# Kernel tuning notes

Hardware: AMD Instinct MI355X
Metric: run time of the kernel (lower is better)

The kernel has to match this reference:

```python
import jax, jax.numpy as jnp
import numpy as np

B, T, C = 2, 2048, 1024
H = 16


def setup_inputs() -> dict:
    key = jax.random.key(0)
    k1, k2, k3 = jax.random.split(key, 3)
    X = jax.random.normal(k1, (B, T, C), dtype=jnp.float32)
    # scale weights like typical inits to keep activations sane
    W_qkv = jax.random.normal(k2, (C, 3 * C), dtype=jnp.float32) / np.sqrt(C)
    W_proj = jax.random.normal(k3, (C, C), dtype=jnp.float32) / np.sqrt(C)
    return {"X": X, "W_qkv": W_qkv, "W_proj": W_proj}


def reference(X, W_qkv, W_proj):
    b, t, c = X.shape
    hd = c // H  # head dim
    qkv = X @ W_qkv  # (B,T,3C)
    q, k, v = jnp.split(qkv, 3, axis=2)
    # (B,H,T,hd)
    q = q.reshape(b, t, H, hd).transpose(0, 2, 1, 3)
    k = k.reshape(b, t, H, hd).transpose(0, 2, 1, 3)
    v = v.reshape(b, t, H, hd).transpose(0, 2, 1, 3)
    att = jnp.einsum("bhqd,bhkd->bhqk", q, k) * (1.0 / np.sqrt(hd))
    causal = jnp.tril(jnp.ones((t, t), dtype=bool))[None, None]
    att = jnp.where(causal, att, -jnp.inf)
    att = jax.nn.softmax(att, axis=-1)
    y = jnp.einsum("bhqk,bhkd->bhqd", att, v)
    y = y.transpose(0, 2, 1, 3).reshape(b, t, c)
    return y @ W_proj
```

## Files before the change

### kernel.cpp

```cpp
#include <hip/hip_runtime.h>
#include <hip/hip_bf16.h>

typedef __attribute__((ext_vector_type(8))) short bf16x8;
typedef __attribute__((ext_vector_type(4))) float f32x4;

#define LOG2E 1.4426950408889634f

__device__ __forceinline__ unsigned short f2b(float f) {
  union { float f; unsigned u; } v; v.f = f;
  unsigned r = v.u + 0x7fffu + ((v.u >> 16) & 1u);
  return (unsigned short)(r >> 16);
}

__device__ __forceinline__ unsigned pack2(float a, float b) {
  __hip_bfloat162 h = __float22bfloat162_rn(make_float2(a, b));
  union { __hip_bfloat162 h; unsigned u; } v;
  v.h = h;
  return v.u;
}

__global__ void cast_x_kernel(const float* __restrict__ X, unsigned short* __restrict__ Xb, int n4) {
  int i = blockIdx.x * blockDim.x + threadIdx.x;
  if (i < n4) {
    float4 v = reinterpret_cast<const float4*>(X)[i];
    ushort4 o = make_ushort4(f2b(v.x), f2b(v.y), f2b(v.z), f2b(v.w));
    reinterpret_cast<ushort4*>(Xb)[i] = o;
  }
}

__global__ void transpose_cast_kernel(const float* __restrict__ W, unsigned short* __restrict__ Wt,
                                      int K, int N) {
  int lane = threadIdx.x & 63;
  int wave = threadIdx.x >> 6;
  int n = blockIdx.x * 64 + lane;
  int k0 = blockIdx.y * 32 + wave * 8;
  bf16x8 v;
#pragma unroll
  for (int j = 0; j < 8; ++j) v[j] = (short)f2b(W[(size_t)(k0 + j) * N + n]);
  *reinterpret_cast<bf16x8*>(&Wt[(size_t)n * K + k0]) = v;
}

__device__ __forceinline__ void stage_tile(const unsigned short* __restrict__ A,
                                           const unsigned short* __restrict__ Bt,
                                           int m0, int n0, int kk, int K,
                                           unsigned short* As, unsigned short* Bs, int tid) {
  int wave = tid >> 6;
  int row = tid >> 2;
  int chunk = tid & 3;
  typedef __attribute__((address_space(3))) unsigned int lds_u32;
  typedef const __attribute__((address_space(1))) unsigned int glb_u32;
  const unsigned short* ga0 = A + (size_t)(m0 + row) * K + kk + chunk * 8;
  const unsigned short* ga1 = A + (size_t)(m0 + 64 + row) * K + kk + chunk * 8;
  const unsigned short* gb0 = Bt + (size_t)(n0 + row) * K + kk + chunk * 8;
  const unsigned short* gb1 = Bt + (size_t)(n0 + 64 + row) * K + kk + chunk * 8;
  __builtin_amdgcn_global_load_lds((glb_u32*)ga0, (lds_u32*)(As + wave * 512), 16, 0, 0);
  __builtin_amdgcn_global_load_lds((glb_u32*)ga1, (lds_u32*)(As + 2048 + wave * 512), 16, 0, 0);
  __builtin_amdgcn_global_load_lds((glb_u32*)gb0, (lds_u32*)(Bs + wave * 512), 16, 0, 0);
  __builtin_amdgcn_global_load_lds((glb_u32*)gb1, (lds_u32*)(Bs + 2048 + wave * 512), 16, 0, 0);
}

template <int MODE>
__launch_bounds__(256, 2)
__global__ void gemm_bt_kernel(const unsigned short* __restrict__ A,
                               const unsigned short* __restrict__ Bt,
                               void* __restrict__ Cout,
                               unsigned short* __restrict__ Vt,
                               int M, int N, int K) {
  __shared__ __align__(16) unsigned short As[2][128 * 32];
  __shared__ __align__(16) unsigned short Bs[2][128 * 32];
  const int tid = threadIdx.x;
  const int lane = tid & 63;
  const int wave = tid >> 6;
  const int wr = wave >> 1, wc = wave & 1;
  const int m0 = blockIdx.y * 128;
  const int n0 = blockIdx.x * 128;
  const int lr = lane & 15;
  const int lk = (lane >> 4) * 8;

  f32x4 zero = {0.f, 0.f, 0.f, 0.f};
  f32x4 acc[4][4];
#pragma unroll
  for (int i = 0; i < 4; ++i)
#pragma unroll
    for (int j = 0; j < 4; ++j) acc[i][j] = zero;

  const int KT = K >> 5;
  stage_tile(A, Bt, m0, n0, 0, K, As[0], Bs[0], tid);
  int buf = 0;
  for (int kt = 0; kt < KT; ++kt) {
    __syncthreads();
    if (kt + 1 < KT) stage_tile(A, Bt, m0, n0, (kt + 1) << 5, K, As[buf ^ 1], Bs[buf ^ 1], tid);
    bf16x8 af[4], bfr[4];
#pragma unroll
    for (int mf = 0; mf < 4; ++mf)
      af[mf] = *reinterpret_cast<const bf16x8*>(&As[buf][(wr * 64 + mf * 16 + lr) * 32 + lk]);
#pragma unroll
    for (int nf = 0; nf < 4; ++nf)
      bfr[nf] = *reinterpret_cast<const bf16x8*>(&Bs[buf][(wc * 64 + nf * 16 + lr) * 32 + lk]);
#pragma unroll
    for (int mf = 0; mf < 4; ++mf)
#pragma unroll
      for (int nf = 0; nf < 4; ++nf)
        acc[mf][nf] = __builtin_amdgcn_mfma_f32_16x16x32_bf16(af[mf], bfr[nf], acc[mf][nf], 0, 0, 0);
    buf ^= 1;
  }

  const int lj = (lane >> 4) * 4;
  if (MODE == 1) {
    float* C = (float*)Cout;
#pragma unroll
    for (int mf = 0; mf < 4; ++mf)
#pragma unroll
      for (int nf = 0; nf < 4; ++nf) {
        int n = n0 + wc * 64 + nf * 16 + lr;
#pragma unroll
        for (int j = 0; j < 4; ++j) {
          int m = m0 + wr * 64 + mf * 16 + lj + j;
          C[(size_t)m * N + n] = acc[mf][nf][j];
        }
      }
  } else {
    unsigned short* QK = (unsigned short*)Cout;
    if (n0 < 2048) {
#pragma unroll
      for (int mf = 0; mf < 4; ++mf)
#pragma unroll
        for (int nf = 0; nf < 4; ++nf) {
          int n = n0 + wc * 64 + nf * 16 + lr;
          float scale = (n < 1024) ? 0.125f : 1.0f;
#pragma unroll
          for (int j = 0; j < 4; ++j) {
            int m = m0 + wr * 64 + mf * 16 + lj + j;
            QK[(size_t)m * 2048 + n] = f2b(acc[mf][nf][j] * scale);
          }
        }
    } else {
#pragma unroll
      for (int mf = 0; mf < 4; ++mf)
#pragma unroll
        for (int nf = 0; nf < 4; ++nf) {
          int n = n0 - 2048 + wc * 64 + nf * 16 + lr;
          int d = n & 63, h = n >> 6;
          int mbase = m0 + wr * 64 + mf * 16 + lj;
          int bb = mbase >> 11, t = mbase & 2047;
          ushort4 v = make_ushort4(f2b(acc[mf][nf][0]), f2b(acc[mf][nf][1]),
                                   f2b(acc[mf][nf][2]), f2b(acc[mf][nf][3]));
          *reinterpret_cast<ushort4*>(&Vt[(((size_t)bb * 16 + h) * 64 + d) * 2048 + t]) = v;
        }
    }
  }
}

#define PFENCE() asm volatile("s_waitcnt lgkmcnt(0)" ::: "memory")

#define KLOAD(TK)                                                                                 \
  {                                                                                               \
    const unsigned short* kp = Kbase + (size_t)((TK) << 6) * 2048;                                \
    _Pragma("unroll")                                                                             \
    for (int nf = 0; nf < 4; ++nf) {                                                              \
      const unsigned short* kq = kp + (size_t)(nf * 16) * 2048;                                   \
      kf[nf][0] = *reinterpret_cast<const bf16x8*>(kq);                                           \
      kf[nf][1] = *reinterpret_cast<const bf16x8*>(kq + 32);                                      \
    }                                                                                             \
  }

#define VLOADX(VF, TK)                                                                            \
  {                                                                                               \
    const unsigned short* vp0 = Vbase + ((TK) << 6);                                              \
    _Pragma("unroll")                                                                             \
    for (int mf = 0; mf < 4; ++mf) {                                                              \
      const unsigned short* vp = vp0 + (size_t)(mf * 16) * 2048;                                  \
      VF[mf][0] = *reinterpret_cast<const bf16x8*>(vp);                                           \
      VF[mf][1] = *reinterpret_cast<const bf16x8*>(vp + 32);                                      \
    }                                                                                             \
  }

#define QKC(ST, QF)                                                                               \
  {                                                                                               \
    __builtin_amdgcn_s_setprio(1);                                                                \
    _Pragma("unroll")                                                                             \
    for (int nf = 0; nf < 4; ++nf) {                                                              \
      ST[nf] = __builtin_amdgcn_mfma_f32_16x16x32_bf16(kf[nf][0], QF[0], zero, 0, 0, 0);          \
      ST[nf] = __builtin_amdgcn_mfma_f32_16x16x32_bf16(kf[nf][1], QF[1], ST[nf], 0, 0, 0);        \
    }                                                                                             \
    __builtin_amdgcn_s_setprio(0);                                                                \
  }

#define MASKST(ST, NFD)                                                                           \
  {                                                                                               \
    _Pragma("unroll")                                                                             \
    for (int nf = 0; nf < 4; ++nf)                                                                \
      _Pragma("unroll")                                                                           \
      for (int j = 0; j < 4; ++j) {                                                               \
        bool kill = (nf > (NFD)) || ((nf == (NFD)) && (4 * lhi + j > lr));                        \
        ST[nf][j] = kill ? -1e30f : ST[nf][j];                                                    \
      }                                                                                           \
  }

#define SMP(ST, MROW, LSUM, ACCO, WOUT)                                                           \
  {                                                                                               \
    float pmax = -1e30f;                                                                          \
    _Pragma("unroll")                                                                             \
    for (int nf = 0; nf < 4; ++nf)                                                                \
      _Pragma("unroll")                                                                           \
      for (int j = 0; j < 4; ++j) pmax = fmaxf(pmax, ST[nf][j]);                                  \
    pmax = fmaxf(pmax, __shfl_xor(pmax, 16));                                                     \
    pmax = fmaxf(pmax, __shfl_xor(pmax, 32));                                                     \
    const float mnew = fmaxf(MROW, pmax);                                                         \
    const float fsc = exp2f((MROW - mnew) * LOG2E);                                               \
    float psum = 0.f;                                                                             \
    _Pragma("unroll")                                                                             \
    for (int nf = 0; nf < 4; ++nf)                                                                \
      _Pragma("unroll")                                                                           \
      for (int h2 = 0; h2 < 2; ++h2) {                                                            \
        float p0 = exp2f((ST[nf][2 * h2] - mnew) * LOG2E);                                        \
        float p1 = exp2f((ST[nf][2 * h2 + 1] - mnew) * LOG2E);                                    \
        psum += p0 + p1;                                                                          \
        WOUT[nf * 2 + h2] = pack2(p0, p1);                                                        \
      }                                                                                           \
    psum += __shfl_xor(psum, 16);                                                                 \
    psum += __shfl_xor(psum, 32);                                                                 \
    LSUM = LSUM * fsc + psum;                                                                     \
    MROW = mnew;                                                                                  \
    _Pragma("unroll")                                                                             \
    for (int mf = 0; mf < 4; ++mf)                                                                \
      _Pragma("unroll")                                                                           \
      for (int j = 0; j < 4; ++j) ACCO[mf][j] *= fsc;                                             \
  }

#define PWRITE(PW, WIN)                                                                           \
  {                                                                                               \
    uint4 w0 = make_uint4(WIN[0], WIN[1], WIN[2], WIN[3]);                                        \
    uint4 w1 = make_uint4(WIN[4], WIN[5], WIN[6], WIN[7]);                                        \
    *reinterpret_cast<uint4*>(&PW[lr][8 * lhi]) = w0;                                             \
    *reinterpret_cast<uint4*>(&PW[lr][8 * lhi + 4]) = w1;                                         \
  }

#define PREAD(PW, PB)                                                                             \
  {                                                                                               \
    _Pragma("unroll")                                                                             \
    for (int kd = 0; kd < 2; ++kd) {                                                              \
      const int nfk = 2 * kd + (lhi >> 1);                                                        \
      const int c = 2 * (nfk & 1) + 4 * (nfk >> 1);                                               \
      const int s0 = 8 * ((2 * lhi) & 3) + c;                                                     \
      const int s1 = 8 * ((2 * lhi + 1) & 3) + c;                                                 \
      union { bf16x8 v; unsigned int u[4]; } pu;                                                  \
      uint2 ra = *reinterpret_cast<const uint2*>(&PW[lr][s0]);                                    \
      uint2 rb = *reinterpret_cast<const uint2*>(&PW[lr][s1]);                                    \
      pu.u[0] = ra.x; pu.u[1] = ra.y; pu.u[2] = rb.x; pu.u[3] = rb.y;                             \
      PB[kd] = pu.v;                                                                              \
    }                                                                                             \
  }

#define PVC(ACCO, VF, PB)                                                                         \
  {                                                                                               \
    __builtin_amdgcn_s_setprio(1);                                                                \
    _Pragma("unroll")                                                                             \
    for (int mf = 0; mf < 4; ++mf) {                                                              \
      ACCO[mf] = __builtin_amdgcn_mfma_f32_16x16x32_bf16(VF[mf][0], PB[0], ACCO[mf], 0, 0, 0);    \
      ACCO[mf] = __builtin_amdgcn_mfma_f32_16x16x32_bf16(VF[mf][1], PB[1], ACCO[mf], 0, 0, 0);    \
    }                                                                                             \
    __builtin_amdgcn_s_setprio(0);                                                                \
  }

#define EPILOG(ACCO, LSUM, Q0)                                                                    \
  {                                                                                               \
    const float inv = 1.0f / LSUM;                                                                \
    unsigned short* Op = O + ((size_t)(b * T + (Q0) + lr)) * 1024 + h * 64 + 4 * lhi;             \
    _Pragma("unroll")                                                                             \
    for (int mf = 0; mf < 4; ++mf) {                                                              \
      uint2 o = make_uint2(pack2(ACCO[mf][0] * inv, ACCO[mf][1] * inv),                           \
                           pack2(ACCO[mf][2] * inv, ACCO[mf][3] * inv));                          \
      *reinterpret_cast<uint2*>(Op + 16 * mf) = o;                                                \
    }                                                                                             \
  }

__launch_bounds__(64)
__global__ void attn_kernel(const unsigned short* __restrict__ QK,
                            const unsigned short* __restrict__ Vt,
                            unsigned short* __restrict__ O) {
  __shared__ unsigned int Pw[2][2][16][36];
  const int T = 2048;
  const int lane = threadIdx.x;
  const int lr = lane & 15;
  const int lhi = lane >> 4;
  const int bh = blockIdx.x & 31;
  const int pid = blockIdx.x >> 5;
  const int b = bh >> 4, h = bh & 15;
  const int qsA = 127 - pid, qsB = pid;
  const int q0A = qsA * 16, q0B = qsB * 16;
  const int ktmaxA = qsA >> 2, ktmaxB = qsB >> 2;
  const int nfdA = qsA & 3, nfdB = qsB & 3;

  const f32x4 zero = {0.f, 0.f, 0.f, 0.f};

  const unsigned short* QpA = QK + ((size_t)(b * T + q0A + lr)) * 2048 + h * 64 + lhi * 8;
  const unsigned short* QpB = QK + ((size_t)(b * T + q0B + lr)) * 2048 + h * 64 + lhi * 8;
  bf16x8 qfA[2] = {*reinterpret_cast<const bf16x8*>(QpA),
                   *reinterpret_cast<const bf16x8*>(QpA + 32)};
  bf16x8 qfB[2] = {*reinterpret_cast<const bf16x8*>(QpB),
                   *reinterpret_cast<const bf16x8*>(QpB + 32)};

  const unsigned short* Kbase = QK + ((size_t)(b * T + lr)) * 2048 + 1024 + h * 64 + lhi * 8;
  const unsigned short* Vbase = Vt + ((size_t)(bh * 64 + lr)) * 2048 + lhi * 8;

  bf16x8 kf[4][2];
  KLOAD(0);

  f32x4 accA[4] = {zero, zero, zero, zero};
  f32x4 accB[4] = {zero, zero, zero, zero};
  float mrowA = -1e30f, lsumA = 0.f, mrowB = -1e30f, lsumB = 0.f;

  for (int kt = 0; kt <= ktmaxA; ++kt) {
    const bool actB = (kt <= ktmaxB);
    const int pp = kt & 1;
    bf16x8 vf[4][2];
    VLOADX(vf, kt);

    f32x4 stA[4], stB[4];
    QKC(stA, qfA);
    if (actB) QKC(stB, qfB);
    {
      int tk = (kt + 1 > ktmaxA) ? ktmaxA : kt + 1;
      KLOAD(tk);
    }
    if (kt == ktmaxA) MASKST(stA, nfdA);
    if (actB && kt == ktmaxB) MASKST(stB, nfdB);

    unsigned WA[8], WB[8];
    SMP(stA, mrowA, lsumA, accA, WA);
    if (actB) SMP(stB, mrowB, lsumB, accB, WB);

    PWRITE(Pw[0][pp], WA);
    if (actB) PWRITE(Pw[1][pp], WB);
    PFENCE();
    bf16x8 pbA[2], pbB[2];
    PREAD(Pw[0][pp], pbA);
    if (actB) PREAD(Pw[1][pp], pbB);

    PVC(accA, vf, pbA);
    if (actB) PVC(accB, vf, pbB);
  }

  EPILOG(accA, lsumA, q0A);
  EPILOG(accB, lsumB, q0B);
}

extern "C" void kernel_launch(void* const* d_in, const int* in_sizes, int n_in,
                              void* d_out, int out_size, void* d_ws, size_t ws_size,
                              hipStream_t stream) {
  const float* X = (const float*)d_in[0];
  const float* Wqkv = (const float*)d_in[1];
  const float* Wproj = (const float*)d_in[2];
  float* out = (float*)d_out;

  char* ws = (char*)d_ws;
  unsigned short* Xb     = (unsigned short*)(ws);
  unsigned short* WqkvT  = (unsigned short*)(ws + 8388608);
  unsigned short* WprojT = (unsigned short*)(ws + 14680064);
  unsigned short* QKb    = (unsigned short*)(ws + 16777216);
  unsigned short* Vt     = (unsigned short*)(ws + 33554432);
  unsigned short* Ob     = (unsigned short*)(ws + 41943040);

  cast_x_kernel<<<4096, 256, 0, stream>>>(X, Xb, 4194304 / 4);
  transpose_cast_kernel<<<dim3(48, 32), 256, 0, stream>>>(Wqkv, WqkvT, 1024, 3072);
  transpose_cast_kernel<<<dim3(16, 32), 256, 0, stream>>>(Wproj, WprojT, 1024, 1024);
  gemm_bt_kernel<0><<<dim3(24, 32), 256, 0, stream>>>(Xb, WqkvT, QKb, Vt, 4096, 3072, 1024);
  attn_kernel<<<2048, 64, 0, stream>>>(QKb, Vt, Ob);
  gemm_bt_kernel<1><<<dim3(8, 32), 256, 0, stream>>>(Ob, WprojT, out, nullptr, 4096, 1024, 1024);
}
```

Measured before the change: 169.5 us.

## Pair adjacent query tiles per attention block, heaviest blocks first

Each attention block now handles two adjacent 16-row query tiles (2j, 2j+1) instead of a mirrored pair (127-p, p). Both tiles share one key-tile range, so the per-iteration actB branches disappear and both tiles run every step, sharing the K and V fragment loads. Blocks are ordered so the longest causal rows launch first. This gives up the balanced per-block work of the mirrored pairing, making blocks uneven, and relies on launch ordering to keep the tail short.

```diff
diff --git a/kernel.cpp b/kernel.cpp
--- a/kernel.cpp
+++ b/kernel.cpp
@@ -263,18 +263,6 @@
     __builtin_amdgcn_s_setprio(0);                                                                \
   }
 
-#define EPILOG(ACCO, LSUM, Q0)                                                                    \
-  {                                                                                               \
-    const float inv = 1.0f / LSUM;                                                                \
-    unsigned short* Op = O + ((size_t)(b * T + (Q0) + lr)) * 1024 + h * 64 + 4 * lhi;             \
-    _Pragma("unroll")                                                                             \
-    for (int mf = 0; mf < 4; ++mf) {                                                              \
-      uint2 o = make_uint2(pack2(ACCO[mf][0] * inv, ACCO[mf][1] * inv),                           \
-                           pack2(ACCO[mf][2] * inv, ACCO[mf][3] * inv));                          \
-      *reinterpret_cast<uint2*>(Op + 16 * mf) = o;                                                \
-    }                                                                                             \
-  }
-
 __launch_bounds__(64)
 __global__ void attn_kernel(const unsigned short* __restrict__ QK,
                             const unsigned short* __restrict__ Vt,
@@ -285,11 +273,11 @@
   const int lr = lane & 15;
   const int lhi = lane >> 4;
   const int bh = blockIdx.x & 31;
-  const int pid = blockIdx.x >> 5;
+  const int j = 63 - (blockIdx.x >> 5);
   const int b = bh >> 4, h = bh & 15;
-  const int qsA = 127 - pid, qsB = pid;
+  const int qsA = 2 * j + 1, qsB = 2 * j;
   const int q0A = qsA * 16, q0B = qsB * 16;
-  const int ktmaxA = qsA >> 2, ktmaxB = qsB >> 2;
+  const int ktmax = (qsB >> 2);
   const int nfdA = qsA & 3, nfdB = qsB & 3;
 
   const f32x4 zero = {0.f, 0.f, 0.f, 0.f};
@@ -311,39 +299,58 @@
   f32x4 accB[4] = {zero, zero, zero, zero};
   float mrowA = -1e30f, lsumA = 0.f, mrowB = -1e30f, lsumB = 0.f;
 
-  for (int kt = 0; kt <= ktmaxA; ++kt) {
-    const bool actB = (kt <= ktmaxB);
+  for (int kt = 0; kt <= ktmax; ++kt) {
     const int pp = kt & 1;
     bf16x8 vf[4][2];
     VLOADX(vf, kt);
 
     f32x4 stA[4], stB[4];
     QKC(stA, qfA);
-    if (actB) QKC(stB, qfB);
+    QKC(stB, qfB);
     {
-      int tk = (kt + 1 > ktmaxA) ? ktmaxA : kt + 1;
+      int tk = (kt + 1 > ktmax) ? ktmax : kt + 1;
       KLOAD(tk);
     }
-    if (kt == ktmaxA) MASKST(stA, nfdA);
-    if (actB && kt == ktmaxB) MASKST(stB, nfdB);
+    if (kt == ktmax) {
+      MASKST(stA, nfdA);
+      MASKST(stB, nfdB);
+    }
 
     unsigned WA[8], WB[8];
     SMP(stA, mrowA, lsumA, accA, WA);
-    if (actB) SMP(stB, mrowB, lsumB, accB, WB);
+    SMP(stB, mrowB, lsumB, accB, WB);
 
     PWRITE(Pw[0][pp], WA);
-    if (actB) PWRITE(Pw[1][pp], WB);
+    PWRITE(Pw[1][pp], WB);
     PFENCE();
     bf16x8 pbA[2], pbB[2];
     PREAD(Pw[0][pp], pbA);
-    if (actB) PREAD(Pw[1][pp], pbB);
+    PREAD(Pw[1][pp], pbB);
 
     PVC(accA, vf, pbA);
-    if (actB) PVC(accB, vf, pbB);
-  }
-
-  EPILOG(accA, lsumA, q0A);
-  EPILOG(accB, lsumB, q0B);
+    PVC(accB, vf, pbB);
+  }
+
+  {
+    const float inv = 1.0f / lsumA;
+    unsigned short* Op = O + ((size_t)(b * T + q0A + lr)) * 1024 + h * 64 + 4 * lhi;
+#pragma unroll
+    for (int mf = 0; mf < 4; ++mf) {
+      uint2 o = make_uint2(pack2(accA[mf][0] * inv, accA[mf][1] * inv),
+                           pack2(accA[mf][2] * inv, accA[mf][3] * inv));
+      *reinterpret_cast<uint2*>(Op + 16 * mf) = o;
+    }
+  }
+  {
+    const float inv = 1.0f / lsumB;
+    unsigned short* Op = O + ((size_t)(b * T + q0B + lr)) * 1024 + h * 64 + 4 * lhi;
+#pragma unroll
+    for (int mf = 0; mf < 4; ++mf) {
+      uint2 o = make_uint2(pack2(accB[mf][0] * inv, accB[mf][1] * inv),
+                           pack2(accB[mf][2] * inv, accB[mf][3] * inv));
+      *reinterpret_cast<uint2*>(Op + 16 * mf) = o;
+    }
+  }
 }
 
 extern "C" void kernel_launch(void* const* d_in, const int* in_sizes, int n_in,
```

Result: faster. 151.4 us (-10.7%).
